# Kernel tuning notes

Measured on AMD Instinct MI355X. Metric: run time of the kernel, lower is better.

## Reference

```python
import jax, jax.numpy as jnp
import numpy as np

N_NODES = 50000
N_EDGES = 800000
D = 128
N_LAYERS = 4
N_GRAPHS = 512
N_CLASS = 10


def setup_inputs() -> dict:
    key = jax.random.key(0)
    ks = jax.random.split(key, 12)
    x = jax.random.normal(ks[0], (N_NODES, D), dtype=jnp.float32)
    edge_index = jax.random.randint(ks[1], (2, N_EDGES), 0, N_NODES, dtype=jnp.int64)
    batch = jnp.sort(jax.random.randint(ks[2], (N_NODES,), 0, N_GRAPHS, dtype=jnp.int64))
    s = 1.0 / np.sqrt(D)
    W_conv = jax.random.uniform(ks[3], (N_LAYERS, D, D), jnp.float32, -s, s)
    b_conv = jnp.zeros((N_LAYERS, D), jnp.float32)
    W1 = jax.random.uniform(ks[4], (D, D), jnp.float32, -s, s)
    b1 = jnp.zeros((D,), jnp.float32)
    W2 = jax.random.uniform(ks[5], (D, D // 2), jnp.float32, -s, s)
    b2 = jnp.zeros((D // 2,), jnp.float32)
    W3 = jax.random.uniform(ks[6], (D // 2, N_CLASS), jnp.float32, -1.0 / np.sqrt(D // 2), 1.0 / np.sqrt(D // 2))
    b3 = jnp.zeros((N_CLASS,), jnp.float32)
    return {"x": x, "edge_index": edge_index, "batch": batch,
            "W_conv": W_conv, "b_conv": b_conv,
            "W1": W1, "b1": b1, "W2": W2, "b2": b2, "W3": W3, "b3": b3}


def reference(x, edge_index, batch, W_conv, b_conv, W1, b1, W2, b2, W3, b3):
    row, col = edge_index[0], edge_index[1]  # messages: source=row -> target=col
    # GCN symmetric normalization with self-loops (PyG GCNConv default).
    deg = jax.ops.segment_sum(jnp.ones((row.shape[0],), x.dtype), col, num_segments=N_NODES) + 1.0
    dinv = jax.lax.rsqrt(deg)
    edge_norm = (dinv[row] * dinv[col])[:, None]      # [E,1]
    self_norm = (1.0 / deg)[:, None]                  # [N,1] = dinv_i * dinv_i

    def gcn_layer(h, W, b):
        h = h @ W                                      # [N,D]
        agg = jax.ops.segment_sum(h[row] * edge_norm, col, num_segments=N_NODES)
        agg = agg + h * self_norm                      # self-loop contribution
        return jax.nn.relu(agg + b)

    h = x
    for l in range(N_LAYERS):
        h = gcn_layer(h, W_conv[l], b_conv[l])

    # global_add_pool over graph ids
    g = jax.ops.segment_sum(h, batch, num_segments=N_GRAPHS)  # [G,D]

    # MLP head (dropout is identity in eval mode)
    g = jax.nn.relu(g @ W1 + b1)
    g = jax.nn.relu(g @ W2 + b2)
    return g @ W3 + b3
```

## Files before the change

kernel.cpp:

```cpp
#include <hip/hip_runtime.h>
#include <stdint.h>
#include <stddef.h>

#define NN 50000
#define NE 800000
#define DD 128
#define NL 4
#define NG 512
#define NC 10
#define NB 196
#define BCAP 5056
#define GPB 49

using short8 = __attribute__((ext_vector_type(8))) short;
using f32x4  = __attribute__((ext_vector_type(4))) float;

__device__ __forceinline__ float bf2f(unsigned short u) {
  union { unsigned int i; float f; } c; c.i = ((unsigned int)u) << 16; return c.f;
}
__device__ __forceinline__ unsigned short f2bf(float f) {
  union { unsigned int i; float f; } c; c.f = f;
  unsigned int i = c.i;
  return (unsigned short)((i + 0x7FFFu + ((i >> 16) & 1u)) >> 16);
}
__device__ __forceinline__ unsigned int pack2(float a, float b) {
  return (unsigned int)f2bf(a) | ((unsigned int)f2bf(b) << 16);
}
__device__ __forceinline__ void acc8(float* a, uint4 p) {
  a[0] += bf2f((unsigned short)(p.x & 0xffffu)); a[1] += bf2f((unsigned short)(p.x >> 16));
  a[2] += bf2f((unsigned short)(p.y & 0xffffu)); a[3] += bf2f((unsigned short)(p.y >> 16));
  a[4] += bf2f((unsigned short)(p.z & 0xffffu)); a[5] += bf2f((unsigned short)(p.z >> 16));
  a[6] += bf2f((unsigned short)(p.w & 0xffffu)); a[7] += bf2f((unsigned short)(p.w >> 16));
}

__global__ __launch_bounds__(1024) void p1b_k(const int* __restrict__ erow,
                                              const int* __restrict__ ecol,
                                              int* __restrict__ cursor,
                                              unsigned int* __restrict__ ebuf) {
  __shared__ int lcnt[256], loff[256];
  __shared__ int gb[NB];
  __shared__ unsigned int stage[4096];
  __shared__ int gpos[4096];
  int tid = threadIdx.x;
  if (tid < 256) lcnt[tid] = 0;
  __syncthreads();
  int e0 = blockIdx.x * 4096 + tid;
  int bk[4], sl[4]; unsigned int pk[4];
#pragma unroll
  for (int j = 0; j < 4; ++j) {
    int e = e0 + j * 1024;
    bk[j] = -1;
    if (e < NE) {
      int d = ecol[e], s = erow[e];
      bk[j] = d >> 8;
      pk[j] = ((unsigned int)(d & 255) << 16) | (unsigned int)s;
      sl[j] = atomicAdd(&lcnt[bk[j]], 1);
    }
  }
  __syncthreads();
  if (tid < 256) loff[tid] = lcnt[tid];
  __syncthreads();
  for (int off = 1; off < 256; off <<= 1) {
    int v = (tid < 256 && tid >= off) ? loff[tid - off] : 0;
    __syncthreads();
    if (tid < 256) loff[tid] += v;
    __syncthreads();
  }
  if (tid < NB) {
    int c = lcnt[tid];
    gb[tid] = c ? atomicAdd(&cursor[tid], c) : 0;
  }
  __syncthreads();
#pragma unroll
  for (int j = 0; j < 4; ++j)
    if (bk[j] >= 0) {
      int ex = loff[bk[j]] - lcnt[bk[j]] + sl[j];
      stage[ex] = pk[j];
      gpos[ex] = bk[j] * BCAP + gb[bk[j]] + sl[j];
    }
  __syncthreads();
  int total = loff[255];
  for (int i = tid; i < total; i += 1024)
    ebuf[gpos[i]] = stage[i];
}

__global__ __launch_bounds__(1024) void p2_k(const unsigned int* __restrict__ ebuf,
                                             const int* __restrict__ cursor,
                                             const float* __restrict__ x,
                                             const int* __restrict__ batch,
                                             const float* __restrict__ Wc,
                                             int* __restrict__ csr_ptr,
                                             int* __restrict__ csr_end,
                                             int* __restrict__ csr_src,
                                             float* __restrict__ dinv,
                                             unsigned short* __restrict__ xb,
                                             int* __restrict__ gptr,
                                             unsigned short* __restrict__ Wbt) {
  int b = blockIdx.x, tid = threadIdx.x;
  if (b >= NB + GPB) {
    int l = b - NB - GPB;
    const float* W = Wc + (size_t)l * DD * DD;
    unsigned short* WT = Wbt + (size_t)l * DD * DD;
    for (int i = tid; i < DD * DD; i += 1024) {
      int n = i >> 7, k = i & 127;
      WT[n * DD + k] = f2bf(W[k * DD + n]);
    }
    return;
  }
  if (b >= NB) {
    int i = (b - NB) * 1024 + tid;
    if (i >= NN) return;
    int bb = batch[i];
    int bp = (i == 0) ? -1 : batch[i - 1];
    for (int g = bp + 1; g <= bb; ++g) gptr[g] = i;
    if (i == NN - 1) { for (int g = bb + 1; g <= NG; ++g) gptr[g] = NN; }
    return;
  }

  __shared__ unsigned int pr[BCAP];
  __shared__ int srcb[BCAP];
  __shared__ int hist_s[256], scn[256], lcur[256];
  __shared__ float dinv_s[256];
  size_t beg = (size_t)b * BCAP;
  int cnt = cursor[b];
  if (cnt > BCAP) cnt = BCAP;

  if (tid < 256) hist_s[tid] = 0;
  __syncthreads();
  for (int i = tid; i < cnt; i += 1024) {
    unsigned int p = ebuf[beg + i];
    pr[i] = p;
    atomicAdd(&hist_s[p >> 16], 1);
  }
  __syncthreads();
  if (tid < 256) scn[tid] = hist_s[tid];
  __syncthreads();
  for (int off = 1; off < 256; off <<= 1) {
    int v = (tid < 256 && tid >= off) ? scn[tid - off] : 0;
    __syncthreads();
    if (tid < 256) scn[tid] += v;
    __syncthreads();
  }
  if (tid < 256) {
    int ex = scn[tid] - hist_s[tid];
    lcur[tid] = ex;
    int V = b * 256 + tid;
    if (V < NN) {
      csr_ptr[V] = (int)beg + ex;
      csr_end[V] = (int)beg + scn[tid];
      float dv = rsqrtf((float)(hist_s[tid] + 1));
      dinv[V] = dv;
      dinv_s[tid] = dv;
    }
  }
  __syncthreads();
  for (int i = tid; i < cnt; i += 1024) {
    unsigned int p = pr[i];
    int pos = atomicAdd(&lcur[p >> 16], 1);
    srcb[pos] = (int)(p & 0xFFFFu);
  }
  __syncthreads();
  for (int i = tid; i < cnt; i += 1024) csr_src[beg + i] = srcb[i];

  for (int i4 = tid; i4 < 256 * 32; i4 += 1024) {
    int vl = i4 >> 5;
    int V = b * 256 + vl;
    if (V < NN) {
      float d = dinv_s[vl];
      int q = i4 & 31;
      f32x4 vx = *((const f32x4*)(x + (size_t)V * DD) + q);
      uint2 o;
      o.x = pack2(vx[0] * d, vx[1] * d);
      o.y = pack2(vx[2] * d, vx[3] * d);
      ((uint2*)(xb + (size_t)V * DD))[q] = o;
    }
  }
}

__global__ __launch_bounds__(1024, 8) void flayer_k(
    const unsigned short* __restrict__ hs,
    const unsigned short* __restrict__ Wb,
    const float* __restrict__ bias,
    unsigned short* __restrict__ out,
    const float* __restrict__ dscale,
    const int* __restrict__ csr_ptr,
    const int* __restrict__ csr_end,
    const int* __restrict__ csr_src,
    const float* __restrict__ dinv) {
  __shared__ unsigned short Wt[128][136];
  __shared__ unsigned short At[16][136];

  int tid = threadIdx.x;
  for (int i = tid; i < 128 * 16; i += 1024) {
    int rr = i >> 4, c = i & 15;
    *(uint4*)&Wt[rr][c * 8] = *(const uint4*)(Wb + rr * DD + c * 8);
  }

  int wave = tid >> 6, lane = tid & 63;
  int qg = lane >> 4, r = lane & 15;
  int v = blockIdx.x * 16 + wave;
  const uint4* rows = (const uint4*)hs;

  float a[8] = {0.f, 0.f, 0.f, 0.f, 0.f, 0.f, 0.f, 0.f};
  float b[8] = {0.f, 0.f, 0.f, 0.f, 0.f, 0.f, 0.f, 0.f};
  if (qg == 0) acc8(a, rows[(size_t)v * 16 + r]);

  int e = csr_ptr[v] + qg, end = csr_end[v];
  for (; e + 12 < end; e += 16) {
    int s0 = csr_src[e];
    int s1 = csr_src[e + 4];
    int s2 = csr_src[e + 8];
    int s3 = csr_src[e + 12];
    uint4 p0 = rows[(size_t)s0 * 16 + r];
    uint4 p1 = rows[(size_t)s1 * 16 + r];
    uint4 p2 = rows[(size_t)s2 * 16 + r];
    uint4 p3 = rows[(size_t)s3 * 16 + r];
    acc8(a, p0); acc8(b, p1); acc8(a, p2); acc8(b, p3);
  }
  for (; e + 4 < end; e += 8) {
    int s0 = csr_src[e];
    int s1 = csr_src[e + 4];
    uint4 p0 = rows[(size_t)s0 * 16 + r];
    uint4 p1 = rows[(size_t)s1 * 16 + r];
    acc8(a, p0); acc8(b, p1);
  }
  if (e < end) acc8(a, rows[(size_t)csr_src[e] * 16 + r]);

#pragma unroll
  for (int t = 0; t < 8; ++t) a[t] += b[t];
#pragma unroll
  for (int t = 0; t < 8; ++t) {
    a[t] += __shfl_xor(a[t], 16, 64);
    a[t] += __shfl_xor(a[t], 32, 64);
  }

  if (qg == 0) {
    float dv = dinv[v];
    uint4 o;
    o.x = pack2(dv * a[0], dv * a[1]);
    o.y = pack2(dv * a[2], dv * a[3]);
    o.z = pack2(dv * a[4], dv * a[5]);
    o.w = pack2(dv * a[6], dv * a[7]);
    *(uint4*)&At[wave][r * 8] = o;
  }
  __syncthreads();

  if (wave < 8) {
    short8 afrag[4];
#pragma unroll
    for (int ks = 0; ks < 4; ++ks)
      afrag[ks] = *(const short8*)&At[r][ks * 32 + qg * 8];

    f32x4 acc = (f32x4){0.f, 0.f, 0.f, 0.f};
#pragma unroll
    for (int ks = 0; ks < 4; ++ks) {
      short8 bfrag = *(const short8*)(&Wt[wave * 16 + r][ks * 32 + qg * 8]);
      acc = __builtin_amdgcn_mfma_f32_16x16x32_bf16(afrag[ks], bfrag, acc, 0, 0, 0);
    }

    int orow = blockIdx.x * 16 + qg * 4;
    int coln = wave * 16 + r;
    float bc = bias[coln];
#pragma unroll
    for (int reg = 0; reg < 4; ++reg) {
      int rr = orow + reg;
      float sc = dscale ? dscale[rr] : 1.f;
      float val = fmaxf(acc[reg] + bc, 0.f) * sc;
      out[(size_t)rr * DD + coln] = f2bf(val);
    }
  }
}

__global__ __launch_bounds__(512) void poolmlp_k(const unsigned short* __restrict__ h,
                                                 const int* __restrict__ gptr,
                                                 const float* __restrict__ W1,
                                                 const float* __restrict__ b1,
                                                 const float* __restrict__ W2,
                                                 const float* __restrict__ b2,
                                                 const float* __restrict__ W3,
                                                 const float* __restrict__ b3,
                                                 float* __restrict__ out) {
  __shared__ float s_part[4][128];
  __shared__ float s_g[128], s_h1[128], s_h2[64];
  int g = blockIdx.x, tid = threadIdx.x;
  int j = tid >> 7, t = tid & 127;
  int beg = gptr[g], end = gptr[g + 1];
  float acc = 0.f;
  for (int v = beg + j; v < end; v += 4) acc += bf2f(h[(size_t)v * DD + t]);
  s_part[j][t] = acc;
  __syncthreads();
  if (tid < 128) {
    s_g[t] = s_part[0][t] + s_part[1][t] + s_part[2][t] + s_part[3][t];
  }
  __syncthreads();
  if (tid < 128) {
    float a = b1[t];
    for (int k = 0; k < 128; ++k) a += s_g[k] * W1[k * 128 + t];
    s_h1[t] = fmaxf(a, 0.f);
  }
  __syncthreads();
  if (tid < 64) {
    float a = b2[t];
    for (int k = 0; k < 128; ++k) a += s_h1[k] * W2[k * 64 + t];
    s_h2[t] = fmaxf(a, 0.f);
  }
  __syncthreads();
  if (tid < NC) {
    float a = b3[t];
    for (int k = 0; k < 64; ++k) a += s_h2[k] * W3[k * NC + t];
    out[g * NC + t] = a;
  }
}


extern "C" void kernel_launch(void* const* d_in, const int* in_sizes, int n_in,
                              void* d_out, int out_size, void* d_ws, size_t ws_size,
                              hipStream_t stream) {
  const float* x     = (const float*)d_in[0];
  const int*   ei    = (const int*)d_in[1];
  const int*   batch = (const int*)d_in[2];
  const float* Wc    = (const float*)d_in[3];
  const float* bc    = (const float*)d_in[4];
  const float* W1    = (const float*)d_in[5];
  const float* b1    = (const float*)d_in[6];
  const float* W2    = (const float*)d_in[7];
  const float* b2    = (const float*)d_in[8];
  const float* W3    = (const float*)d_in[9];
  const float* b3    = (const float*)d_in[10];
  float* out = (float*)d_out;

  const int* erow = ei;
  const int* ecol = ei + NE;

  char* w = (char*)d_ws;
  int*   cursor  = (int*)w;    w += NB * 4;
  int*   csr_ptr = (int*)w;    w += (size_t)(NN + 4) * 4;
  int*   csr_end = (int*)w;    w += (size_t)(NN + 4) * 4;
  int*   gptr    = (int*)w;    w += (NG + 4) * 4;
  int*   csr_src = (int*)w;    w += (size_t)NB * BCAP * 4;
  float* dinv    = (float*)w;  w += (size_t)NN * 4;
  w = (char*)(((uintptr_t)w + 255) & ~(uintptr_t)255);
  unsigned short* Wbt  = (unsigned short*)w; w += (size_t)NL * DD * DD * 2;
  unsigned short* xb   = (unsigned short*)w; w += (size_t)NN * DD * 2;
  unsigned short* hA   = (unsigned short*)w; w += (size_t)NN * DD * 2;
  unsigned short* hB   = (unsigned short*)w; w += (size_t)NN * DD * 2;
  unsigned int* ebuf = (unsigned int*)hA;

  hipMemsetAsync(cursor, 0, NB * 4, stream);

  p1b_k<<<NB, 1024, 0, stream>>>(erow, ecol, cursor, ebuf);
  p2_k <<<NB + GPB + NL, 1024, 0, stream>>>(ebuf, cursor, x, batch, Wc, csr_ptr,
                                            csr_end, csr_src, dinv, xb, gptr, Wbt);

  const int fGrid = NN / 16;

  for (int l = 0; l < NL; ++l) {
    const unsigned short* hin = (l == 0) ? xb : ((l & 1) ? hA : hB);
    unsigned short* dst = (l & 1) ? hB : hA;
    const float* dsc = (l == NL - 1) ? nullptr : dinv;
    flayer_k<<<fGrid, 1024, 0, stream>>>(hin, Wbt + (size_t)l * DD * DD,
                                         bc + (size_t)l * DD, dst, dsc,
                                         csr_ptr, csr_end, csr_src, dinv);
  }

  poolmlp_k<<<NG, 512, 0, stream>>>(hB, gptr, W1, b1, W2, b2, W3, b3, out);

  (void)in_sizes; (void)n_in; (void)out_size; (void)ws_size;
}
```

Baseline: 301.4 us.

## Balance edge aggregation across waves with packed dst ids and LDS atomics

The CSR source entries now keep the local destination id in their upper 16 bits. Each block's 16 destination nodes share one contiguous edge range, which is split evenly across waves and quarter-waves instead of one wave per node. Runs of edges with the same destination are accumulated in registers and flushed with float atomics into a shared fp32 tile, then scaled and converted to bf16 for the MFMA. This targets load imbalance from the varying node degrees, at the cost of LDS atomics, an extra barrier and a larger shared footprint. The pooling kernel is also changed to read rows as 16-byte vectors and reduce them with shuffles.

```diff
diff --git a/kernel.cpp b/kernel.cpp
--- a/kernel.cpp
+++ b/kernel.cpp
@@ -157,7 +157,7 @@
   for (int i = tid; i < cnt; i += 1024) {
     unsigned int p = pr[i];
     int pos = atomicAdd(&lcur[p >> 16], 1);
-    srcb[pos] = (int)(p & 0xFFFFu);
+    srcb[pos] = (int)p;
   }
   __syncthreads();
   for (int i = tid; i < cnt; i += 1024) csr_src[beg + i] = srcb[i];
@@ -188,7 +188,8 @@
     const int* __restrict__ csr_src,
     const float* __restrict__ dinv) {
   __shared__ unsigned short Wt[128][136];
-  __shared__ unsigned short At[16][136];
+  __shared__ float At32[16][128];
+  __shared__ unsigned short Atb[16][136];
 
   int tid = threadIdx.x;
   for (int i = tid; i < 128 * 16; i += 1024) {
@@ -198,50 +199,57 @@
 
   int wave = tid >> 6, lane = tid & 63;
   int qg = lane >> 4, r = lane & 15;
-  int v = blockIdx.x * 16 + wave;
+  int v0 = blockIdx.x * 16;
+  int tb = v0 & 255;
   const uint4* rows = (const uint4*)hs;
 
-  float a[8] = {0.f, 0.f, 0.f, 0.f, 0.f, 0.f, 0.f, 0.f};
-  float b[8] = {0.f, 0.f, 0.f, 0.f, 0.f, 0.f, 0.f, 0.f};
-  if (qg == 0) acc8(a, rows[(size_t)v * 16 + r]);
-
-  int e = csr_ptr[v] + qg, end = csr_end[v];
-  for (; e + 12 < end; e += 16) {
-    int s0 = csr_src[e];
-    int s1 = csr_src[e + 4];
-    int s2 = csr_src[e + 8];
-    int s3 = csr_src[e + 12];
-    uint4 p0 = rows[(size_t)s0 * 16 + r];
-    uint4 p1 = rows[(size_t)s1 * 16 + r];
-    uint4 p2 = rows[(size_t)s2 * 16 + r];
-    uint4 p3 = rows[(size_t)s3 * 16 + r];
-    acc8(a, p0); acc8(b, p1); acc8(a, p2); acc8(b, p3);
-  }
-  for (; e + 4 < end; e += 8) {
-    int s0 = csr_src[e];
-    int s1 = csr_src[e + 4];
-    uint4 p0 = rows[(size_t)s0 * 16 + r];
-    uint4 p1 = rows[(size_t)s1 * 16 + r];
-    acc8(a, p0); acc8(b, p1);
-  }
-  if (e < end) acc8(a, rows[(size_t)csr_src[e] * 16 + r]);
-
-#pragma unroll
-  for (int t = 0; t < 8; ++t) a[t] += b[t];
-#pragma unroll
-  for (int t = 0; t < 8; ++t) {
-    a[t] += __shfl_xor(a[t], 16, 64);
-    a[t] += __shfl_xor(a[t], 32, 64);
-  }
-
   if (qg == 0) {
-    float dv = dinv[v];
-    uint4 o;
-    o.x = pack2(dv * a[0], dv * a[1]);
-    o.y = pack2(dv * a[2], dv * a[3]);
-    o.z = pack2(dv * a[4], dv * a[5]);
-    o.w = pack2(dv * a[6], dv * a[7]);
-    *(uint4*)&At[wave][r * 8] = o;
+    uint4 sp = rows[(size_t)(v0 + wave) * 16 + r];
+    float s8[8] = {0.f, 0.f, 0.f, 0.f, 0.f, 0.f, 0.f, 0.f};
+    acc8(s8, sp);
+    *(f32x4*)&At32[wave][r * 8]     = (f32x4){s8[0], s8[1], s8[2], s8[3]};
+    *(f32x4*)&At32[wave][r * 8 + 4] = (f32x4){s8[4], s8[5], s8[6], s8[7]};
+  }
+  __syncthreads();
+
+  int beg  = csr_ptr[v0];
+  int endt = csr_end[v0 + 15];
+  int len  = endt - beg;
+  int w0 = beg + (int)(((long long)len * wave) >> 4);
+  int w1 = beg + (int)(((long long)len * (wave + 1)) >> 4);
+  int qlen = w1 - w0;
+  int q0 = w0 + (int)(((long long)qlen * qg) >> 2);
+  int q1 = w0 + (int)(((long long)qlen * (qg + 1)) >> 2);
+
+  float A[8] = {0.f, 0.f, 0.f, 0.f, 0.f, 0.f, 0.f, 0.f};
+  int cur = -1;
+  for (int e = q0; e < q1; ++e) {
+    unsigned int p = (unsigned int)csr_src[e];
+    int dl = (int)(p >> 16) - tb;
+    if (dl != cur) {
+      if (cur >= 0) {
+#pragma unroll
+        for (int j = 0; j < 8; ++j) atomicAdd(&At32[cur][r * 8 + j], A[j]);
+      }
+      cur = dl;
+#pragma unroll
+      for (int j = 0; j < 8; ++j) A[j] = 0.f;
+    }
+    uint4 row = rows[(size_t)(p & 0xffffu) * 16 + r];
+    acc8(A, row);
+  }
+  if (cur >= 0) {
+#pragma unroll
+    for (int j = 0; j < 8; ++j) atomicAdd(&At32[cur][r * 8 + j], A[j]);
+  }
+  __syncthreads();
+
+  {
+    int i4 = tid;
+    int row = i4 >> 6, c2 = (i4 & 63) * 2;
+    float dv = dinv[v0 + row];
+    unsigned int o = pack2(At32[row][c2] * dv, At32[row][c2 + 1] * dv);
+    *(unsigned int*)&Atb[row][c2] = o;
   }
   __syncthreads();
 
@@ -249,7 +257,7 @@
     short8 afrag[4];
 #pragma unroll
     for (int ks = 0; ks < 4; ++ks)
-      afrag[ks] = *(const short8*)&At[r][ks * 32 + qg * 8];
+      afrag[ks] = *(const short8*)&Atb[r][ks * 32 + qg * 8];
 
     f32x4 acc = (f32x4){0.f, 0.f, 0.f, 0.f};
 #pragma unroll
@@ -258,7 +266,7 @@
       acc = __builtin_amdgcn_mfma_f32_16x16x32_bf16(afrag[ks], bfrag, acc, 0, 0, 0);
     }
 
-    int orow = blockIdx.x * 16 + qg * 4;
+    int orow = v0 + qg * 4;
     int coln = wave * 16 + r;
     float bc = bias[coln];
 #pragma unroll
@@ -280,35 +288,50 @@
                                                  const float* __restrict__ W3,
                                                  const float* __restrict__ b3,
                                                  float* __restrict__ out) {
-  __shared__ float s_part[4][128];
+  __shared__ float s_part[8][128];
   __shared__ float s_g[128], s_h1[128], s_h2[64];
   int g = blockIdx.x, tid = threadIdx.x;
-  int j = tid >> 7, t = tid & 127;
+  int wave = tid >> 6, lane = tid & 63;
+  int qg = lane >> 4, r = lane & 15;
   int beg = gptr[g], end = gptr[g + 1];
-  float acc = 0.f;
-  for (int v = beg + j; v < end; v += 4) acc += bf2f(h[(size_t)v * DD + t]);
-  s_part[j][t] = acc;
+  const uint4* rows = (const uint4*)h;
+
+  float A[8] = {0.f, 0.f, 0.f, 0.f, 0.f, 0.f, 0.f, 0.f};
+  for (int v = beg + wave * 4 + qg; v < end; v += 32)
+    acc8(A, rows[(size_t)v * 16 + r]);
+#pragma unroll
+  for (int j = 0; j < 8; ++j) {
+    A[j] += __shfl_xor(A[j], 16, 64);
+    A[j] += __shfl_xor(A[j], 32, 64);
+  }
+  if (qg == 0) {
+    *(f32x4*)&s_part[wave][r * 8]     = (f32x4){A[0], A[1], A[2], A[3]};
+    *(f32x4*)&s_part[wave][r * 8 + 4] = (f32x4){A[4], A[5], A[6], A[7]};
+  }
   __syncthreads();
   if (tid < 128) {
-    s_g[t] = s_part[0][t] + s_part[1][t] + s_part[2][t] + s_part[3][t];
+    float sg = 0.f;
+#pragma unroll
+    for (int w = 0; w < 8; ++w) sg += s_part[w][tid];
+    s_g[tid] = sg;
   }
   __syncthreads();
   if (tid < 128) {
-    float a = b1[t];
-    for (int k = 0; k < 128; ++k) a += s_g[k] * W1[k * 128 + t];
-    s_h1[t] = fmaxf(a, 0.f);
+    float a = b1[tid];
+    for (int k = 0; k < 128; ++k) a += s_g[k] * W1[k * 128 + tid];
+    s_h1[tid] = fmaxf(a, 0.f);
   }
   __syncthreads();
   if (tid < 64) {
-    float a = b2[t];
-    for (int k = 0; k < 128; ++k) a += s_h1[k] * W2[k * 64 + t];
-    s_h2[t] = fmaxf(a, 0.f);
+    float a = b2[tid];
+    for (int k = 0; k < 128; ++k) a += s_h1[k] * W2[k * 64 + tid];
+    s_h2[tid] = fmaxf(a, 0.f);
   }
   __syncthreads();
   if (tid < NC) {
-    float a = b3[t];
-    for (int k = 0; k < 64; ++k) a += s_h2[k] * W3[k * NC + t];
-    out[g * NC + t] = a;
+    float a = b3[tid];
+    for (int k = 0; k < 64; ++k) a += s_h2[k] * W3[k * NC + tid];
+    out[g * NC + tid] = a;
   }
 }
 
```

Result: slower. 854.8 us (+183.6%).

## Sort nodes by in-degree to balance per-block gather work; vectorize pooling

Applied to the files above, without the earlier changes.

Computes each node's in-degree histogram during CSR build and adds a new kernel that counting-sorts nodes by degree into a permutation. Each layer kernel then processes nodes in permuted order, so the 16 waves of a block have similar edge counts and less idle time waiting on the slowest wave. Output rows are scattered back to the original node index, which costs the contiguous write locality. The pooling kernel is also changed to read 16-byte vectors per lane, reducing partial sums with shuffles across 8 waves.

```diff
diff --git a/kernel.cpp b/kernel.cpp
--- a/kernel.cpp
+++ b/kernel.cpp
@@ -95,7 +95,9 @@
                                              float* __restrict__ dinv,
                                              unsigned short* __restrict__ xb,
                                              int* __restrict__ gptr,
-                                             unsigned short* __restrict__ Wbt) {
+                                             unsigned short* __restrict__ Wbt,
+                                             int* __restrict__ deg,
+                                             int* __restrict__ dhist) {
   int b = blockIdx.x, tid = threadIdx.x;
   if (b >= NB + GPB) {
     int l = b - NB - GPB;
@@ -151,6 +153,9 @@
       float dv = rsqrtf((float)(hist_s[tid] + 1));
       dinv[V] = dv;
       dinv_s[tid] = dv;
+      int dg = hist_s[tid];
+      deg[V] = dg;
+      atomicAdd(&dhist[dg > 255 ? 255 : dg], 1);
     }
   }
   __syncthreads();
@@ -177,6 +182,30 @@
   }
 }
 
+__global__ __launch_bounds__(1024) void p3_k(const int* __restrict__ deg,
+                                             const int* __restrict__ dhist,
+                                             int* __restrict__ gcur,
+                                             int* __restrict__ perm) {
+  __shared__ int incl[256], exb[256];
+  int tid = threadIdx.x;
+  if (tid < 256) incl[tid] = dhist[tid];
+  __syncthreads();
+  for (int off = 1; off < 256; off <<= 1) {
+    int v = (tid < 256 && tid >= off) ? incl[tid - off] : 0;
+    __syncthreads();
+    if (tid < 256) incl[tid] += v;
+    __syncthreads();
+  }
+  if (tid < 256) exb[tid] = incl[tid] - dhist[tid];
+  __syncthreads();
+  int i = blockIdx.x * 1024 + tid;
+  if (i < NN) {
+    int bn = deg[i]; if (bn > 255) bn = 255;
+    int pos = exb[bn] + atomicAdd(&gcur[bn], 1);
+    perm[pos] = i;
+  }
+}
+
 __global__ __launch_bounds__(1024, 8) void flayer_k(
     const unsigned short* __restrict__ hs,
     const unsigned short* __restrict__ Wb,
@@ -186,9 +215,11 @@
     const int* __restrict__ csr_ptr,
     const int* __restrict__ csr_end,
     const int* __restrict__ csr_src,
-    const float* __restrict__ dinv) {
+    const float* __restrict__ dinv,
+    const int* __restrict__ perm) {
   __shared__ unsigned short Wt[128][136];
   __shared__ unsigned short At[16][136];
+  __shared__ int s_vid[16];
 
   int tid = threadIdx.x;
   for (int i = tid; i < 128 * 16; i += 1024) {
@@ -198,7 +229,8 @@
 
   int wave = tid >> 6, lane = tid & 63;
   int qg = lane >> 4, r = lane & 15;
-  int v = blockIdx.x * 16 + wave;
+  int v = perm[blockIdx.x * 16 + wave];
+  if (lane == 0) s_vid[wave] = v;
   const uint4* rows = (const uint4*)hs;
 
   float a[8] = {0.f, 0.f, 0.f, 0.f, 0.f, 0.f, 0.f, 0.f};
@@ -258,15 +290,14 @@
       acc = __builtin_amdgcn_mfma_f32_16x16x32_bf16(afrag[ks], bfrag, acc, 0, 0, 0);
     }
 
-    int orow = blockIdx.x * 16 + qg * 4;
     int coln = wave * 16 + r;
     float bc = bias[coln];
 #pragma unroll
     for (int reg = 0; reg < 4; ++reg) {
-      int rr = orow + reg;
-      float sc = dscale ? dscale[rr] : 1.f;
+      int vr = s_vid[qg * 4 + reg];
+      float sc = dscale ? dscale[vr] : 1.f;
       float val = fmaxf(acc[reg] + bc, 0.f) * sc;
-      out[(size_t)rr * DD + coln] = f2bf(val);
+      out[(size_t)vr * DD + coln] = f2bf(val);
     }
   }
 }
@@ -280,35 +311,50 @@
                                                  const float* __restrict__ W3,
                                                  const float* __restrict__ b3,
                                                  float* __restrict__ out) {
-  __shared__ float s_part[4][128];
+  __shared__ float s_part[8][128];
   __shared__ float s_g[128], s_h1[128], s_h2[64];
   int g = blockIdx.x, tid = threadIdx.x;
-  int j = tid >> 7, t = tid & 127;
+  int wave = tid >> 6, lane = tid & 63;
+  int qg = lane >> 4, r = lane & 15;
   int beg = gptr[g], end = gptr[g + 1];
-  float acc = 0.f;
-  for (int v = beg + j; v < end; v += 4) acc += bf2f(h[(size_t)v * DD + t]);
-  s_part[j][t] = acc;
+  const uint4* rows = (const uint4*)h;
+
+  float A[8] = {0.f, 0.f, 0.f, 0.f, 0.f, 0.f, 0.f, 0.f};
+  for (int v = beg + wave * 4 + qg; v < end; v += 32)
+    acc8(A, rows[(size_t)v * 16 + r]);
+#pragma unroll
+  for (int j = 0; j < 8; ++j) {
+    A[j] += __shfl_xor(A[j], 16, 64);
+    A[j] += __shfl_xor(A[j], 32, 64);
+  }
+  if (qg == 0) {
+    *(f32x4*)&s_part[wave][r * 8]     = (f32x4){A[0], A[1], A[2], A[3]};
+    *(f32x4*)&s_part[wave][r * 8 + 4] = (f32x4){A[4], A[5], A[6], A[7]};
+  }
   __syncthreads();
   if (tid < 128) {
-    s_g[t] = s_part[0][t] + s_part[1][t] + s_part[2][t] + s_part[3][t];
+    float sg = 0.f;
+#pragma unroll
+    for (int w = 0; w < 8; ++w) sg += s_part[w][tid];
+    s_g[tid] = sg;
   }
   __syncthreads();
   if (tid < 128) {
-    float a = b1[t];
-    for (int k = 0; k < 128; ++k) a += s_g[k] * W1[k * 128 + t];
-    s_h1[t] = fmaxf(a, 0.f);
+    float a = b1[tid];
+    for (int k = 0; k < 128; ++k) a += s_g[k] * W1[k * 128 + tid];
+    s_h1[tid] = fmaxf(a, 0.f);
   }
   __syncthreads();
   if (tid < 64) {
-    float a = b2[t];
-    for (int k = 0; k < 128; ++k) a += s_h1[k] * W2[k * 64 + t];
-    s_h2[t] = fmaxf(a, 0.f);
+    float a = b2[tid];
+    for (int k = 0; k < 128; ++k) a += s_h1[k] * W2[k * 64 + tid];
+    s_h2[tid] = fmaxf(a, 0.f);
   }
   __syncthreads();
   if (tid < NC) {
-    float a = b3[t];
-    for (int k = 0; k < 64; ++k) a += s_h2[k] * W3[k * NC + t];
-    out[g * NC + t] = a;
+    float a = b3[tid];
+    for (int k = 0; k < 64; ++k) a += s_h2[k] * W3[k * NC + tid];
+    out[g * NC + tid] = a;
   }
 }
 
@@ -334,6 +380,10 @@
 
   char* w = (char*)d_ws;
   int*   cursor  = (int*)w;    w += NB * 4;
+  int*   dhist   = (int*)w;    w += 256 * 4;
+  int*   gcur    = (int*)w;    w += 256 * 4;
+  int*   deg     = (int*)w;    w += (size_t)(NN + 4) * 4;
+  int*   perm    = (int*)w;    w += (size_t)(NN + 4) * 4;
   int*   csr_ptr = (int*)w;    w += (size_t)(NN + 4) * 4;
   int*   csr_end = (int*)w;    w += (size_t)(NN + 4) * 4;
   int*   gptr    = (int*)w;    w += (NG + 4) * 4;
@@ -346,11 +396,13 @@
   unsigned short* hB   = (unsigned short*)w; w += (size_t)NN * DD * 2;
   unsigned int* ebuf = (unsigned int*)hA;
 
-  hipMemsetAsync(cursor, 0, NB * 4, stream);
+  hipMemsetAsync(cursor, 0, NB * 4 + 2048, stream);
 
   p1b_k<<<NB, 1024, 0, stream>>>(erow, ecol, cursor, ebuf);
   p2_k <<<NB + GPB + NL, 1024, 0, stream>>>(ebuf, cursor, x, batch, Wc, csr_ptr,
-                                            csr_end, csr_src, dinv, xb, gptr, Wbt);
+                                            csr_end, csr_src, dinv, xb, gptr, Wbt,
+                                            deg, dhist);
+  p3_k <<<GPB, 1024, 0, stream>>>(deg, dhist, gcur, perm);
 
   const int fGrid = NN / 16;
 
@@ -360,7 +412,7 @@
     const float* dsc = (l == NL - 1) ? nullptr : dinv;
     flayer_k<<<fGrid, 1024, 0, stream>>>(hin, Wbt + (size_t)l * DD * DD,
                                          bc + (size_t)l * DD, dst, dsc,
-                                         csr_ptr, csr_end, csr_src, dinv);
+                                         csr_ptr, csr_end, csr_src, dinv, perm);
   }
 
   poolmlp_k<<<NG, 512, 0, stream>>>(hB, gptr, W1, b1, W2, b2, W3, b3, out);
```

Measured after the change: 602.0 us. 99.7% more time.
